# Kernel optimization log

Measured on AMD Instinct MI355X. Metric: run time of the kernel, lower is better.

Reference implementation:

```python
import jax, jax.numpy as jnp
import numpy as np

# Each of the 16 soft logic gates in tableOperator is a polynomial
#   gate_t(A,B) = c0 + cA*A + cB*B + cAB*A*B
# _COEFF[t] = [c0, cA, cB, cAB], matching the torch tableOperator rows 0..15.
_COEFF = np.array([
    [0,  0,  0,  0],   # 0: 0
    [0,  0,  0,  1],   # 1: A*B
    [0,  1,  0, -1],   # 2: A - A*B
    [0,  1,  0,  0],   # 3: A
    [0,  0,  1, -1],   # 4: B - A*B
    [0,  0,  1,  0],   # 5: B
    [0,  1,  1, -2],   # 6: A + B - 2AB
    [0,  1,  1, -1],   # 7: A + B - AB
    [1, -1, -1,  1],   # 8: 1 - (A + B - AB)
    [1, -1, -1,  2],   # 9: 1 - (A + B - 2AB)
    [1,  0, -1,  0],   # 10: 1 - B
    [1,  0, -1,  1],   # 11: 1 - B + AB
    [1, -1,  0,  0],   # 12: 1 - A
    [1, -1,  0,  1],   # 13: 1 - A + AB
    [1,  0,  0, -1],   # 14: 1 - AB
    [1,  0,  0,  0],   # 15: 1
], dtype=np.float32)

PREV_SIZE, SIZE, BATCH = 2048, 2048, 8192

def setup_inputs() -> dict:
    key = jax.random.key(0)
    k1, k2, k3, k4 = jax.random.split(key, 4)
    return {
        "prev_layer_output": jax.random.uniform(k1, (PREV_SIZE, BATCH), dtype=jnp.float32),
        "input_A_weights": jax.random.normal(k2, (SIZE, PREV_SIZE), dtype=jnp.float32) * 0.05,
        "input_B_weights": jax.random.normal(k3, (SIZE, PREV_SIZE), dtype=jnp.float32) * 0.05,
        "table_weights": jax.random.normal(k4, (16, SIZE), dtype=jnp.float32) * 0.05,
    }

def reference(prev_layer_output, input_A_weights, input_B_weights, table_weights):
    # Training (grad-enabled) path of LogicLayer.forward; GradFactor(x, 1) is identity.
    pA = jax.nn.softmax(input_A_weights, axis=1)   # [size, prev_size]
    pB = jax.nn.softmax(input_B_weights, axis=1)   # [size, prev_size]
    pT = jax.nn.softmax(table_weights, axis=0)     # [16, size]
    A = pA @ prev_layer_output                     # [size, batch]
    B = pB @ prev_layer_output                     # [size, batch]
    # Fuse sum_t pT[t] * gate_t(A,B): contract gate coefficients with table probs.
    c = jnp.einsum('tc,ts->cs', jnp.asarray(_COEFF), pT)  # [4, size]
    out = (c[0][:, None]
           + c[1][:, None] * A
           + c[2][:, None] * B
           + c[3][:, None] * (A * B))               # [size, batch]
    return out
```

## Files before the change

kernel.cpp:

```cpp
#include <hip/hip_runtime.h>
#include <hip/hip_bf16.h>

#define M_DIM 2048
#define K_DIM 2048
#define N_DIM 8192

#define BM 128
#define BN 256
#define BK 128
#define NT (K_DIM / BK)

typedef __attribute__((ext_vector_type(4))) int i32x4;

static __device__ __forceinline__ void stage1k(const unsigned char* g, void* l) {
    __builtin_amdgcn_global_load_lds(
        (const __attribute__((address_space(1))) void*)g,
        (__attribute__((address_space(3))) void*)l, 16, 0, 0);
}

__global__ __launch_bounds__(256) void softmax_rows_kernel(
    const float* __restrict__ Wa, const float* __restrict__ Wb,
    unsigned char* __restrict__ Pa, unsigned char* __restrict__ Pb,
    float* __restrict__ SA, float* __restrict__ SB)
{
    const float* W = blockIdx.y ? Wb : Wa;
    unsigned char* P = blockIdx.y ? Pb : Pa;
    float* S = blockIdx.y ? SB : SA;
    const int row = blockIdx.x;
    const int t = threadIdx.x;
    const float* w = W + (size_t)row * K_DIM + t * 8;
    float4 v0 = *(const float4*)(w);
    float4 v1 = *(const float4*)(w + 4);
    float x[8] = {v0.x, v0.y, v0.z, v0.w, v1.x, v1.y, v1.z, v1.w};

    float m = x[0];
#pragma unroll
    for (int i = 1; i < 8; ++i) m = fmaxf(m, x[i]);
#pragma unroll
    for (int off = 32; off >= 1; off >>= 1) m = fmaxf(m, __shfl_xor(m, off));
    __shared__ float redm[4], reds[4];
    const int wid = t >> 6;
    if ((t & 63) == 0) redm[wid] = m;
    __syncthreads();
    m = fmaxf(fmaxf(redm[0], redm[1]), fmaxf(redm[2], redm[3]));

    float s = 0.f;
#pragma unroll
    for (int i = 0; i < 8; ++i) { x[i] = __expf(x[i] - m); s += x[i]; }
#pragma unroll
    for (int off = 32; off >= 1; off >>= 1) s += __shfl_xor(s, off);
    if ((t & 63) == 0) reds[wid] = s;
    __syncthreads();
    s = reds[0] + reds[1] + reds[2] + reds[3];

    union { unsigned char u[8]; int2 v; } pk;
#pragma unroll
    for (int i = 0; i < 8; ++i)
        pk.u[i] = (unsigned char)(int)(127.f * x[i] + 0.5f);
    *(int2*)(P + (size_t)row * K_DIM + t * 8) = pk.v;
    if (t == 0) S[row] = 1.f / (16129.f * s);
}

__global__ __launch_bounds__(256) void table_c_kernel(
    const float* __restrict__ TW, float4* __restrict__ C4)
{
    const int s = blockIdx.x * 256 + threadIdx.x;
    if (s >= M_DIM) return;
    float x[16];
    float m = -1e30f;
#pragma unroll
    for (int t = 0; t < 16; ++t) { x[t] = TW[t * M_DIM + s]; m = fmaxf(m, x[t]); }
    float sum = 0.f;
#pragma unroll
    for (int t = 0; t < 16; ++t) { x[t] = __expf(x[t] - m); sum += x[t]; }
    const float inv = 1.0f / sum;

    const float c0a[16] = {0,0,0,0,0,0,0,0, 1,1,1,1,1,1,1,1};
    const float cAa[16] = {0,0,1,1,0,0,1,1, -1,-1,0,0,-1,-1,0,0};
    const float cBa[16] = {0,0,0,0,1,1,1,1, -1,-1,-1,-1,0,0,0,0};
    const float cXa[16] = {0,1,-1,0,-1,0,-2,-1, 1,2,0,1,0,1,-1,0};
    float c0 = 0.f, cA = 0.f, cB = 0.f, cX = 0.f;
#pragma unroll
    for (int t = 0; t < 16; ++t) {
        const float p = x[t] * inv;
        c0 += p * c0a[t]; cA += p * cAa[t]; cB += p * cBa[t]; cX += p * cXa[t];
    }
    C4[s] = make_float4(c0, cA, cB, cX);
}

__global__ __launch_bounds__(256) void transp_conv_kernel(
    const float* __restrict__ src, unsigned char* __restrict__ dst)
{
    __shared__ unsigned char tile[64][64];
    const int n0 = blockIdx.x * 64;
    const int k0 = blockIdx.y * 64;
    const int t = threadIdx.x;
#pragma unroll
    for (int it = 0; it < 4; ++it) {
        const int lin = it * 256 + t;
        const int k = lin >> 4;
        const int n4 = (lin & 15) * 4;
        float4 v = *(const float4*)(src + (size_t)(k0 + k) * N_DIM + n0 + n4);
        tile[n4 + 0][k] = (unsigned char)(int)(127.f * v.x + 0.5f);
        tile[n4 + 1][k] = (unsigned char)(int)(127.f * v.y + 0.5f);
        tile[n4 + 2][k] = (unsigned char)(int)(127.f * v.z + 0.5f);
        tile[n4 + 3][k] = (unsigned char)(int)(127.f * v.w + 0.5f);
    }
    __syncthreads();
    const int n = t >> 2;
    const int k16 = (t & 3) * 16;
    int4 v = *(const int4*)&tile[n][k16];
    *(int4*)(dst + (size_t)(n0 + n) * K_DIM + k0 + k16) = v;
}


#define MFMA8(ACC, FA, FP, MI0)                                                \
    _Pragma("unroll") for (int mi = (MI0); mi < (MI0) + 2; ++mi)               \
    _Pragma("unroll") for (int ni = 0; ni < 4; ++ni)                           \
        ACC[mi][ni] = __builtin_amdgcn_mfma_i32_16x16x64_i8(                   \
            FA[mi], FP[ni], ACC[mi][ni], 0, 0, 0);

#define STAGE_A(T) do { const int b_ = (T) & 1; const size_t o_ = (size_t)(T) * BK; \
    stage1k(gPa + o_,  &sPa[b_][0][wid * 16][0]);                              \
    stage1k(gPt0 + o_, &sPt[b_][0][wid * 16][0]); } while (0)
#define STAGE_B(T) do { const int b_ = (T) & 1; const size_t o_ = (size_t)(T) * BK; \
    stage1k(gPt1 + o_, &sPt[b_][0][128 + wid * 16][0]);                        \
    stage1k(gPb + o_,  &sPb[b_][0][wid * 16][0]); } while (0)
#define STAGE_C(T) do { const int b_ = (T) & 1; const size_t o_ = (size_t)(T) * BK + 64; \
    stage1k(gPa + o_,  &sPa[b_][1][wid * 16][0]);                              \
    stage1k(gPt0 + o_, &sPt[b_][1][wid * 16][0]); } while (0)
#define STAGE_D(T) do { const int b_ = (T) & 1; const size_t o_ = (size_t)(T) * BK + 64; \
    stage1k(gPt1 + o_, &sPt[b_][1][128 + wid * 16][0]);                        \
    stage1k(gPb + o_,  &sPb[b_][1][wid * 16][0]); } while (0)

__global__ __launch_bounds__(512, 2) void logic_gemm_kernel(
    const unsigned char* __restrict__ Pa,
    const unsigned char* __restrict__ Pb,
    const unsigned char* __restrict__ Pt,
    const float4* __restrict__ C4,
    const float* __restrict__ SA,
    const float* __restrict__ SB,
    float* __restrict__ out)
{
    __shared__ unsigned char sPa[2][2][128][64];
    __shared__ unsigned char sPb[2][2][128][64];
    __shared__ unsigned char sPt[2][2][256][64];

    const int m0 = blockIdx.y * BM;
    const int n0 = blockIdx.x * BN;
    const int t = threadIdx.x;
    const int wid = t >> 6, lane = t & 63;
    const int wr = wid >> 2, wc = wid & 3;
    const int lq = lane >> 4, lr = lane & 15;

    const int srow = lane >> 2;
    const int scol = (((lane & 3) ^ ((lane >> 3) & 3)) << 4);
    const unsigned char* gPa  = Pa + (size_t)(m0 + wid * 16 + srow) * K_DIM + scol;
    const unsigned char* gPb  = Pb + (size_t)(m0 + wid * 16 + srow) * K_DIM + scol;
    const unsigned char* gPt0 = Pt + (size_t)(n0 + wid * 16 + srow) * K_DIM + scol;
    const unsigned char* gPt1 = gPt0 + (size_t)128 * K_DIM;

    const int cswz = (lq ^ ((lr >> 1) & 3)) << 4;
    const int roA = (wr * 64 + lr) * 64 + cswz;
    const int roP = (wc * 64 + lr) * 64 + cswz;

    i32x4 accA[4][4] = {};
    i32x4 accB[4][4] = {};
    i32x4 fX0[4], fX1[4], fpA[4], fpB[4];

    STAGE_A(0); STAGE_B(0); STAGE_C(0); STAGE_D(0);
    STAGE_A(1); STAGE_B(1); STAGE_C(1);
    asm volatile("s_waitcnt vmcnt(10)" ::: "memory");
    __builtin_amdgcn_s_barrier();
#pragma unroll
    for (int i = 0; i < 4; ++i)
        fX0[i] = *(const i32x4*)((const char*)&sPa[0][0][0][0] + roA + i * 1024);
#pragma unroll
    for (int i = 0; i < 4; ++i)
        fpA[i] = *(const i32x4*)((const char*)&sPt[0][0][0][0] + roP + i * 1024);

    for (int kt = 0; kt < NT; ++kt) {
        const int buf = kt & 1;
        const char* bA1 = (const char*)&sPa[buf][1][0][0];
        const char* bB0 = (const char*)&sPb[buf][0][0][0];
        const char* bB1 = (const char*)&sPb[buf][1][0][0];
        const char* bP1 = (const char*)&sPt[buf][1][0][0];
        const char* nA0 = (const char*)&sPa[buf ^ 1][0][0][0];
        const char* nP0 = (const char*)&sPt[buf ^ 1][0][0][0];

        __builtin_amdgcn_s_setprio(1);
        MFMA8(accA, fX0, fpA, 0);
        __builtin_amdgcn_s_setprio(0);
        if (kt < NT - 2) asm volatile("s_waitcnt vmcnt(6)" ::: "memory");
        else             asm volatile("s_waitcnt vmcnt(0)" ::: "memory");
#pragma unroll
        for (int i = 0; i < 4; ++i) fX1[i] = *(const i32x4*)(bB0 + roA + i * 1024);
        if (kt + 1 < NT) STAGE_D(kt + 1);
        __builtin_amdgcn_s_setprio(1);
        MFMA8(accA, fX0, fpA, 2);
        __builtin_amdgcn_s_setprio(0);
        __builtin_amdgcn_s_barrier();

        __builtin_amdgcn_s_setprio(1);
        MFMA8(accB, fX1, fpA, 0);
        __builtin_amdgcn_s_setprio(0);
#pragma unroll
        for (int i = 0; i < 4; ++i) fX0[i] = *(const i32x4*)(bA1 + roA + i * 1024);
#pragma unroll
        for (int i = 0; i < 4; ++i) fpB[i] = *(const i32x4*)(bP1 + roP + i * 1024);
        if (kt + 2 < NT) STAGE_A(kt + 2);
        __builtin_amdgcn_s_setprio(1);
        MFMA8(accB, fX1, fpA, 2);
        __builtin_amdgcn_s_setprio(0);
        __builtin_amdgcn_s_barrier();

        __builtin_amdgcn_s_setprio(1);
        MFMA8(accA, fX0, fpB, 0);
        __builtin_amdgcn_s_setprio(0);
        if (kt < NT - 2) asm volatile("s_waitcnt vmcnt(6)" ::: "memory");
        else             asm volatile("s_waitcnt vmcnt(0)" ::: "memory");
#pragma unroll
        for (int i = 0; i < 4; ++i) fX1[i] = *(const i32x4*)(bB1 + roA + i * 1024);
        if (kt + 2 < NT) STAGE_B(kt + 2);
        __builtin_amdgcn_s_setprio(1);
        MFMA8(accA, fX0, fpB, 2);
        __builtin_amdgcn_s_setprio(0);
        __builtin_amdgcn_s_barrier();

        __builtin_amdgcn_s_setprio(1);
        MFMA8(accB, fX1, fpB, 0);
        __builtin_amdgcn_s_setprio(0);
#pragma unroll
        for (int i = 0; i < 4; ++i) fX0[i] = *(const i32x4*)(nA0 + roA + i * 1024);
#pragma unroll
        for (int i = 0; i < 4; ++i) fpA[i] = *(const i32x4*)(nP0 + roP + i * 1024);
        if (kt + 2 < NT) STAGE_C(kt + 2);
        __builtin_amdgcn_s_setprio(1);
        MFMA8(accB, fX1, fpB, 2);
        __builtin_amdgcn_s_setprio(0);
        __builtin_amdgcn_s_barrier();
    }

#pragma unroll
    for (int mi = 0; mi < 4; ++mi) {
#pragma unroll
        for (int i = 0; i < 4; ++i) {
            const int row = m0 + wr * 64 + mi * 16 + lq * 4 + i;
            const float4 c = C4[row];
            const float sa = SA[row];
            const float sb = SB[row];
#pragma unroll
            for (int ni = 0; ni < 4; ++ni) {
                const int col = n0 + wc * 64 + ni * 16 + lr;
                const float Av = (float)accA[mi][ni][i] * sa;
                const float Bv = (float)accB[mi][ni][i] * sb;
                out[(size_t)row * N_DIM + col] = c.x + c.y * Av + c.z * Bv + c.w * Av * Bv;
            }
        }
    }
}

extern "C" void kernel_launch(void* const* d_in, const int* in_sizes, int n_in,
                              void* d_out, int out_size, void* d_ws, size_t ws_size,
                              hipStream_t stream) {
    const float* prev = (const float*)d_in[0];
    const float* Wa   = (const float*)d_in[1];
    const float* Wb   = (const float*)d_in[2];
    const float* TW   = (const float*)d_in[3];
    float* out = (float*)d_out;

    char* ws = (char*)d_ws;
    unsigned char* Pa = (unsigned char*)(ws);
    unsigned char* Pb = (unsigned char*)(ws + (size_t)(4u << 20));
    unsigned char* Pt = (unsigned char*)(ws + (size_t)(8u << 20));
    float4* C4 = (float4*)(ws + (size_t)(24u << 20));
    float*  SA = (float*)(ws + (size_t)(24u << 20) + (32u << 10));
    float*  SB = (float*)(ws + (size_t)(24u << 20) + (64u << 10));

    softmax_rows_kernel<<<dim3(2048, 2), 256, 0, stream>>>(Wa, Wb, Pa, Pb, SA, SB);
    table_c_kernel<<<dim3(8), 256, 0, stream>>>(TW, C4);
    transp_conv_kernel<<<dim3(N_DIM / 64, K_DIM / 64), 256, 0, stream>>>(prev, Pt);
    logic_gemm_kernel<<<dim3(N_DIM / BN, M_DIM / BM), 512, 0, stream>>>(Pa, Pb, Pt, C4, SA, SB, out);
}
```

Baseline: 91.98 us.

## Load Pa/Pb fragments directly from global into registers, stage only Pt in LDS

The A and B operand fragments are now read straight from global memory into registers in MFMA layout, and the Pa/Pb shared-memory buffers and their staging are removed. Only the shared Pt tile still goes through LDS, which roughly halves LDS traffic and footprint. The cost is that A/B global load latency is exposed to each wave and the loads are uncoalesced 16-byte row chunks. The vmcnt accounting is reworked around the mixed register and LDS loads, and it may be fragile because the register loads are also counted.

```diff
diff --git a/kernel.cpp b/kernel.cpp
--- a/kernel.cpp
+++ b/kernel.cpp
@@ -120,18 +120,20 @@
         ACC[mi][ni] = __builtin_amdgcn_mfma_i32_16x16x64_i8(                   \
             FA[mi], FP[ni], ACC[mi][ni], 0, 0, 0);
 
-#define STAGE_A(T) do { const int b_ = (T) & 1; const size_t o_ = (size_t)(T) * BK; \
-    stage1k(gPa + o_,  &sPa[b_][0][wid * 16][0]);                              \
-    stage1k(gPt0 + o_, &sPt[b_][0][wid * 16][0]); } while (0)
-#define STAGE_B(T) do { const int b_ = (T) & 1; const size_t o_ = (size_t)(T) * BK; \
-    stage1k(gPt1 + o_, &sPt[b_][0][128 + wid * 16][0]);                        \
-    stage1k(gPb + o_,  &sPb[b_][0][wid * 16][0]); } while (0)
-#define STAGE_C(T) do { const int b_ = (T) & 1; const size_t o_ = (size_t)(T) * BK + 64; \
-    stage1k(gPa + o_,  &sPa[b_][1][wid * 16][0]);                              \
-    stage1k(gPt0 + o_, &sPt[b_][1][wid * 16][0]); } while (0)
-#define STAGE_D(T) do { const int b_ = (T) & 1; const size_t o_ = (size_t)(T) * BK + 64; \
-    stage1k(gPt1 + o_, &sPt[b_][1][128 + wid * 16][0]);                        \
-    stage1k(gPb + o_,  &sPb[b_][1][wid * 16][0]); } while (0)
+#define LOAD_FRAGS(SET, GP, T, KH)                                             \
+    _Pragma("unroll") for (int i = 0; i < 4; ++i)                              \
+        SET[i] = *(const i32x4*)((GP) + (size_t)i * 16 * K_DIM +               \
+                                 (size_t)(T) * BK + (KH) * 64);
+
+#define RD_P(BUF, KH)                                                          \
+    _Pragma("unroll") for (int i = 0; i < 4; ++i)                              \
+        fp[i] = *(const i32x4*)((const char*)&sPt[BUF][KH][0][0] + roP + i * 1024);
+
+#define STAGE_P(T, KH) do { if ((T) < NT) {                                    \
+    const int b_ = (T) & 1;                                                    \
+    const size_t o_ = (size_t)(T) * BK + (KH) * 64;                            \
+    stage1k(gPt0 + o_, &sPt[b_][KH][wid * 16][0]);                             \
+    stage1k(gPt1 + o_, &sPt[b_][KH][128 + wid * 16][0]); } } while (0)
 
 __global__ __launch_bounds__(512, 2) void logic_gemm_kernel(
     const unsigned char* __restrict__ Pa,
@@ -142,8 +144,6 @@
     const float* __restrict__ SB,
     float* __restrict__ out)
 {
-    __shared__ unsigned char sPa[2][2][128][64];
-    __shared__ unsigned char sPb[2][2][128][64];
     __shared__ unsigned char sPt[2][2][256][64];
 
     const int m0 = blockIdx.y * BM;
@@ -155,89 +155,60 @@
 
     const int srow = lane >> 2;
     const int scol = (((lane & 3) ^ ((lane >> 3) & 3)) << 4);
-    const unsigned char* gPa  = Pa + (size_t)(m0 + wid * 16 + srow) * K_DIM + scol;
-    const unsigned char* gPb  = Pb + (size_t)(m0 + wid * 16 + srow) * K_DIM + scol;
     const unsigned char* gPt0 = Pt + (size_t)(n0 + wid * 16 + srow) * K_DIM + scol;
     const unsigned char* gPt1 = gPt0 + (size_t)128 * K_DIM;
 
+    const unsigned char* gA = Pa + (size_t)(m0 + wr * 64 + lr) * K_DIM + lq * 16;
+    const unsigned char* gB = Pb + (size_t)(m0 + wr * 64 + lr) * K_DIM + lq * 16;
+
     const int cswz = (lq ^ ((lr >> 1) & 3)) << 4;
-    const int roA = (wr * 64 + lr) * 64 + cswz;
     const int roP = (wc * 64 + lr) * 64 + cswz;
 
     i32x4 accA[4][4] = {};
     i32x4 accB[4][4] = {};
-    i32x4 fX0[4], fX1[4], fpA[4], fpB[4];
-
-    STAGE_A(0); STAGE_B(0); STAGE_C(0); STAGE_D(0);
-    STAGE_A(1); STAGE_B(1); STAGE_C(1);
-    asm volatile("s_waitcnt vmcnt(10)" ::: "memory");
+    i32x4 aA[4], aB[4], fp[4];
+
+    STAGE_P(0, 0); STAGE_P(0, 1); STAGE_P(1, 0); STAGE_P(1, 1);
+    LOAD_FRAGS(aA, gA, 0, 0);
+    LOAD_FRAGS(aB, gB, 0, 0);
+    asm volatile("s_waitcnt vmcnt(8)" ::: "memory");
     __builtin_amdgcn_s_barrier();
-#pragma unroll
-    for (int i = 0; i < 4; ++i)
-        fX0[i] = *(const i32x4*)((const char*)&sPa[0][0][0][0] + roA + i * 1024);
-#pragma unroll
-    for (int i = 0; i < 4; ++i)
-        fpA[i] = *(const i32x4*)((const char*)&sPt[0][0][0][0] + roP + i * 1024);
+    RD_P(0, 0);
 
     for (int kt = 0; kt < NT; ++kt) {
         const int buf = kt & 1;
-        const char* bA1 = (const char*)&sPa[buf][1][0][0];
-        const char* bB0 = (const char*)&sPb[buf][0][0][0];
-        const char* bB1 = (const char*)&sPb[buf][1][0][0];
-        const char* bP1 = (const char*)&sPt[buf][1][0][0];
-        const char* nA0 = (const char*)&sPa[buf ^ 1][0][0][0];
-        const char* nP0 = (const char*)&sPt[buf ^ 1][0][0][0];
-
-        __builtin_amdgcn_s_setprio(1);
-        MFMA8(accA, fX0, fpA, 0);
-        __builtin_amdgcn_s_setprio(0);
-        if (kt < NT - 2) asm volatile("s_waitcnt vmcnt(6)" ::: "memory");
-        else             asm volatile("s_waitcnt vmcnt(0)" ::: "memory");
-#pragma unroll
-        for (int i = 0; i < 4; ++i) fX1[i] = *(const i32x4*)(bB0 + roA + i * 1024);
-        if (kt + 1 < NT) STAGE_D(kt + 1);
-        __builtin_amdgcn_s_setprio(1);
-        MFMA8(accA, fX0, fpA, 2);
-        __builtin_amdgcn_s_setprio(0);
-        __builtin_amdgcn_s_barrier();
-
-        __builtin_amdgcn_s_setprio(1);
-        MFMA8(accB, fX1, fpA, 0);
-        __builtin_amdgcn_s_setprio(0);
-#pragma unroll
-        for (int i = 0; i < 4; ++i) fX0[i] = *(const i32x4*)(bA1 + roA + i * 1024);
-#pragma unroll
-        for (int i = 0; i < 4; ++i) fpB[i] = *(const i32x4*)(bP1 + roP + i * 1024);
-        if (kt + 2 < NT) STAGE_A(kt + 2);
-        __builtin_amdgcn_s_setprio(1);
-        MFMA8(accB, fX1, fpA, 2);
-        __builtin_amdgcn_s_setprio(0);
-        __builtin_amdgcn_s_barrier();
-
-        __builtin_amdgcn_s_setprio(1);
-        MFMA8(accA, fX0, fpB, 0);
-        __builtin_amdgcn_s_setprio(0);
-        if (kt < NT - 2) asm volatile("s_waitcnt vmcnt(6)" ::: "memory");
-        else             asm volatile("s_waitcnt vmcnt(0)" ::: "memory");
-#pragma unroll
-        for (int i = 0; i < 4; ++i) fX1[i] = *(const i32x4*)(bB1 + roA + i * 1024);
-        if (kt + 2 < NT) STAGE_B(kt + 2);
-        __builtin_amdgcn_s_setprio(1);
-        MFMA8(accA, fX0, fpB, 2);
-        __builtin_amdgcn_s_setprio(0);
-        __builtin_amdgcn_s_barrier();
-
-        __builtin_amdgcn_s_setprio(1);
-        MFMA8(accB, fX1, fpB, 0);
-        __builtin_amdgcn_s_setprio(0);
-#pragma unroll
-        for (int i = 0; i < 4; ++i) fX0[i] = *(const i32x4*)(nA0 + roA + i * 1024);
-#pragma unroll
-        for (int i = 0; i < 4; ++i) fpA[i] = *(const i32x4*)(nP0 + roP + i * 1024);
-        if (kt + 2 < NT) STAGE_C(kt + 2);
-        __builtin_amdgcn_s_setprio(1);
-        MFMA8(accB, fX1, fpB, 2);
-        __builtin_amdgcn_s_setprio(0);
+
+        __builtin_amdgcn_s_setprio(1);
+        MFMA8(accA, aA, fp, 0);
+        MFMA8(accA, aA, fp, 2);
+        __builtin_amdgcn_s_setprio(0);
+        LOAD_FRAGS(aA, gA, kt, 1);
+        __builtin_amdgcn_s_barrier();
+
+        __builtin_amdgcn_s_setprio(1);
+        MFMA8(accB, aB, fp, 0);
+        MFMA8(accB, aB, fp, 2);
+        __builtin_amdgcn_s_setprio(0);
+        LOAD_FRAGS(aB, gB, kt, 1);
+        RD_P(buf, 1);
+        STAGE_P(kt + 2, 0);
+        __builtin_amdgcn_s_barrier();
+
+        __builtin_amdgcn_s_setprio(1);
+        MFMA8(accA, aA, fp, 0);
+        MFMA8(accA, aA, fp, 2);
+        __builtin_amdgcn_s_setprio(0);
+        if (kt + 1 < NT) LOAD_FRAGS(aA, gA, kt + 1, 0);
+        __builtin_amdgcn_s_barrier();
+
+        __builtin_amdgcn_s_setprio(1);
+        MFMA8(accB, aB, fp, 0);
+        MFMA8(accB, aB, fp, 2);
+        __builtin_amdgcn_s_setprio(0);
+        if (kt + 1 < NT) LOAD_FRAGS(aB, gB, kt + 1, 0);
+        RD_P(buf ^ 1, 0);
+        STAGE_P(kt + 2, 1);
+        asm volatile("s_waitcnt vmcnt(10)" ::: "memory");
         __builtin_amdgcn_s_barrier();
     }
 
```

New measurement: 164.2 us. 78.5% more time.
